# Kernel tuning notes

Hardware: AMD Instinct MI355X
Metric: run time of the kernel (lower is better)

Reference implementation:

```python
import jax, jax.numpy as jnp
import numpy as np

DIM = 768
HEADS = 12


def setup_inputs() -> dict:
    key = jax.random.key(0)
    ks = jax.random.split(key, 7)
    bs, nmm, nv, na = 32, 256, 196, 60
    s = DIM ** -0.5
    return {
        "xmm": jax.random.normal(ks[0], (bs, nmm, DIM), jnp.float32),
        "xv": jax.random.normal(ks[1], (bs, nv, DIM), jnp.float32),
        "xa": jax.random.normal(ks[2], (bs, na, DIM), jnp.float32),
        "Wq": jax.random.normal(ks[3], (DIM, DIM), jnp.float32) * s,
        "Wkv": jax.random.normal(ks[4], (DIM, 2 * DIM), jnp.float32) * s,
        "Wproj": jax.random.normal(ks[5], (DIM, DIM), jnp.float32) * s,
        "bproj": jnp.zeros((DIM,), jnp.float32),
    }


def reference(xmm, xv, xa, Wq, Wkv, Wproj, bproj):
    bs, nmm, dim = xmm.shape
    hd = dim // HEADS
    scale = hd ** -0.5
    x_src = jnp.concatenate([xv, xa], axis=1)            # [bs, nv+na, dim]
    q = (xmm @ Wq).reshape(bs, nmm, HEADS, hd).transpose(0, 2, 1, 3)   # [b,h,q,d]
    kv = (x_src @ Wkv).reshape(bs, -1, 2, HEADS, hd).transpose(2, 0, 3, 1, 4)
    k, v = kv[0], kv[1]                                  # [b,h,k,d]
    attn = jax.nn.softmax(jnp.einsum('bhqd,bhkd->bhqk', q, k) * scale, axis=-1)
    out = jnp.einsum('bhqk,bhkd->bhqd', attn, v)
    out = out.transpose(0, 2, 1, 3).reshape(bs, nmm, dim)
    out = out @ Wproj + bproj
    return out, attn
```

## Files before the change

### kernel.cpp

```cpp
#include <hip/hip_runtime.h>


typedef __attribute__((ext_vector_type(8))) _Float16 f16x8;
typedef __attribute__((ext_vector_type(4))) _Float16 f16x4;
typedef __attribute__((ext_vector_type(4))) float    f32x4;

#define AS1 __attribute__((address_space(1)))
#define AS3 __attribute__((address_space(3)))

__device__ __forceinline__ void gload_lds16(const void* g, void* l) {
    void* gnc = const_cast<void*>(g);
    __builtin_amdgcn_global_load_lds((AS1 void*)gnc, (AS3 void*)l, 16, 0, 0);
}

__global__ __launch_bounds__(256) void cast_f32_f16(const float* __restrict__ in,
                                                    _Float16* __restrict__ out, int n4) {
    int id = blockIdx.x * 256 + threadIdx.x;
    if (id >= n4) return;
    float4 v = ((const float4*)in)[id];
    f16x4 h = { (_Float16)v.x, (_Float16)v.y, (_Float16)v.z, (_Float16)v.w };
    ((f16x4*)out)[id] = h;
}

__global__ __launch_bounds__(256) void concat_cast(const float* __restrict__ xv,
                                                   const float* __restrict__ xa,
                                                   _Float16* __restrict__ out) {
    int id = blockIdx.x * 256 + threadIdx.x;
    if (id >= 1572864) return;
    int c4 = id % 192;
    int r  = (id / 192) & 255;
    int b  = id / 49152;
    float4 v;
    if (r < 196) v = ((const float4*)xv)[((long)b * 196 + r) * 192 + c4];
    else         v = ((const float4*)xa)[((long)b * 60 + (r - 196)) * 192 + c4];
    f16x4 h = { (_Float16)v.x, (_Float16)v.y, (_Float16)v.z, (_Float16)v.w };
    ((f16x4*)out)[id] = h;
}

__global__ __launch_bounds__(256) void transcast(const float* __restrict__ in,
                                                 _Float16* __restrict__ out, int K, int N) {
    int id = blockIdx.x * 256 + threadIdx.x;
    if (id >= K * N) return;
    int k = id % K, n = id / K;
    out[id] = (_Float16)in[(long)k * N + n];
}

template <int OUT_F32>
__global__ __launch_bounds__(256, 2)
void gemm_bt(const _Float16* __restrict__ A, const _Float16* __restrict__ Bt,
             void* __restrict__ C, const float* __restrict__ bias,
             int M, int N, int K) {
    __shared__ _Float16 As[128 * 64];
    __shared__ _Float16 Bs[128 * 64];

    const int tid  = threadIdx.x;
    const int wave = tid >> 6, lane = tid & 63;
    const int lrow = lane & 15, quad = lane >> 4;
    const long bm = (long)blockIdx.y * 128, bn = (long)blockIdx.x * 128;
    const int wm = (wave >> 1) * 64, wn = (wave & 1) * 64;

    f32x4 acc[4][4];
    const f32x4 fz = {0.f, 0.f, 0.f, 0.f};
#pragma unroll
    for (int mt = 0; mt < 4; ++mt)
#pragma unroll
        for (int nt = 0; nt < 4; ++nt) acc[mt][nt] = fz;

    for (int k0 = 0; k0 < K; k0 += 64) {
#pragma unroll
        for (int it = 0; it < 4; ++it) {
            int seg = tid + it * 256;
            int rr = seg >> 3, pp = seg & 7;
            int cc = ((pp ^ (rr & 7)) << 3);
            gload_lds16(A  + (bm + rr) * (long)K + k0 + cc, As + seg * 8);
            gload_lds16(Bt + (bn + rr) * (long)K + k0 + cc, Bs + seg * 8);
        }
        __syncthreads();
#pragma unroll
        for (int ks = 0; ks < 2; ++ks) {
            f16x8 af[4], bf[4];
#pragma unroll
            for (int mt = 0; mt < 4; ++mt) {
                int r = wm + mt * 16 + lrow;
                af[mt] = *(const f16x8*)(As + r * 64 + (((ks * 4 + quad) ^ (r & 7)) << 3));
            }
#pragma unroll
            for (int nt = 0; nt < 4; ++nt) {
                int r = wn + nt * 16 + lrow;
                bf[nt] = *(const f16x8*)(Bs + r * 64 + (((ks * 4 + quad) ^ (r & 7)) << 3));
            }
#pragma unroll
            for (int mt = 0; mt < 4; ++mt)
#pragma unroll
                for (int nt = 0; nt < 4; ++nt)
                    acc[mt][nt] = __builtin_amdgcn_mfma_f32_16x16x32_f16(
                        af[mt], bf[nt], acc[mt][nt], 0, 0, 0);
        }
        __syncthreads();
    }

#pragma unroll
    for (int mt = 0; mt < 4; ++mt) {
#pragma unroll
        for (int j = 0; j < 4; ++j) {
            long row = bm + wm + mt * 16 + quad * 4 + j;
#pragma unroll
            for (int nt = 0; nt < 4; ++nt) {
                long col = bn + wn + nt * 16 + lrow;
                float v = acc[mt][nt][j];
                if (OUT_F32) ((float*)C)[row * N + col] = v + bias[col];
                else         ((_Float16*)C)[row * N + col] = (_Float16)v;
            }
        }
    }
}

__global__ __launch_bounds__(256, 2)
void attn_kernel(const _Float16* __restrict__ Qg, const _Float16* __restrict__ KVg,
                 float* __restrict__ attn_out, _Float16* __restrict__ Og) {
    __shared__ _Float16 sh[32768];
    _Float16* Ks = sh;
    _Float16* Vt = sh + 16384;
    _Float16* Ps = sh;

    const int tid  = threadIdx.x;
    const int wave = tid >> 6, lane = tid & 63;
    const int lrow = lane & 15, quad = lane >> 4;
    const int qb = blockIdx.x, h = blockIdx.y, b = blockIdx.z;
    const long qrow0 = (long)b * 256 + qb * 64;
    const long krow0 = (long)b * 256;

    f16x8 aq[2];
#pragma unroll
    for (int ks = 0; ks < 2; ++ks)
        aq[ks] = *(const f16x8*)(Qg + (qrow0 + wave * 16 + lrow) * 768 + h * 64 + ks * 32 + quad * 8);

#pragma unroll
    for (int it = 0; it < 8; ++it) {
        int seg = tid + it * 256;
        int rr = seg >> 3, pp = seg & 7;
        int cc = ((pp ^ (rr & 7)) << 3);
        gload_lds16(KVg + (krow0 + rr) * 1536 + h * 64 + cc, Ks + seg * 8);
    }
#pragma unroll
    for (int it = 0; it < 8; ++it) {
        int seg = tid + it * 256;
        int key = seg >> 3, d0 = (seg & 7) * 8;
        f16x8 v = *(const f16x8*)(KVg + (krow0 + key) * 1536 + 768 + h * 64 + d0);
#pragma unroll
        for (int i = 0; i < 8; ++i) {
            int d = d0 + i;
            Vt[d * 256 + ((((key >> 3) ^ (d & 7)) << 3) | (key & 7))] = v[i];
        }
    }
    __syncthreads();

    f32x4 sacc[16];
    const f32x4 fz = {0.f, 0.f, 0.f, 0.f};
#pragma unroll
    for (int nt = 0; nt < 16; ++nt) sacc[nt] = fz;
#pragma unroll
    for (int ks = 0; ks < 2; ++ks) {
#pragma unroll
        for (int nt = 0; nt < 16; ++nt) {
            int r = nt * 16 + lrow;
            f16x8 bk = *(const f16x8*)(Ks + r * 64 + (((ks * 4 + quad) ^ (r & 7)) << 3));
            sacc[nt] = __builtin_amdgcn_mfma_f32_16x16x32_f16(aq[ks], bk, sacc[nt], 0, 0, 0);
        }
    }

    float li[4];
#pragma unroll
    for (int j = 0; j < 4; ++j) {
        float m = -1e30f;
#pragma unroll
        for (int nt = 0; nt < 16; ++nt) { sacc[nt][j] *= 0.125f; m = fmaxf(m, sacc[nt][j]); }
        m = fmaxf(m, __shfl_xor(m, 1));
        m = fmaxf(m, __shfl_xor(m, 2));
        m = fmaxf(m, __shfl_xor(m, 4));
        m = fmaxf(m, __shfl_xor(m, 8));
        float s = 0.f;
#pragma unroll
        for (int nt = 0; nt < 16; ++nt) {
            float p = __expf(sacc[nt][j] - m);
            sacc[nt][j] = p; s += p;
        }
        s += __shfl_xor(s, 1); s += __shfl_xor(s, 2);
        s += __shfl_xor(s, 4); s += __shfl_xor(s, 8);
        li[j] = 1.f / s;
    }
    __syncthreads();

    const long abase = (((long)b * 12 + h) * 256 + qb * 64) * 256;
#pragma unroll
    for (int j = 0; j < 4; ++j) {
        int prow = wave * 16 + quad * 4 + j;
#pragma unroll
        for (int nt = 0; nt < 16; ++nt) {
            int col = nt * 16 + lrow;
            float p = sacc[nt][j];
            Ps[prow * 256 + ((((col >> 3) ^ (prow & 7)) << 3) | (col & 7))] = (_Float16)p;
            attn_out[abase + (long)prow * 256 + col] = p * li[j];
        }
    }
    __syncthreads();

    f32x4 oacc[4];
#pragma unroll
    for (int nt = 0; nt < 4; ++nt) oacc[nt] = fz;
#pragma unroll
    for (int ks = 0; ks < 8; ++ks) {
        int pr = wave * 16 + lrow;
        f16x8 ap = *(const f16x8*)(Ps + pr * 256 + (((ks * 4 + quad) ^ (pr & 7)) << 3));
#pragma unroll
        for (int nt = 0; nt < 4; ++nt) {
            int d = nt * 16 + lrow;
            f16x8 bv = *(const f16x8*)(Vt + d * 256 + (((ks * 4 + quad) ^ (d & 7)) << 3));
            oacc[nt] = __builtin_amdgcn_mfma_f32_16x16x32_f16(ap, bv, oacc[nt], 0, 0, 0);
        }
    }
#pragma unroll
    for (int j = 0; j < 4; ++j) {
        long orow = qrow0 + wave * 16 + quad * 4 + j;
#pragma unroll
        for (int nt = 0; nt < 4; ++nt)
            Og[orow * 768 + h * 64 + nt * 16 + lrow] = (_Float16)(oacc[nt][j] * li[j]);
    }
}

extern "C" void kernel_launch(void* const* d_in, const int* in_sizes, int n_in,
                              void* d_out, int out_size, void* d_ws, size_t ws_size,
                              hipStream_t stream) {
    const float* xmm   = (const float*)d_in[0];
    const float* xv    = (const float*)d_in[1];
    const float* xa    = (const float*)d_in[2];
    const float* Wq    = (const float*)d_in[3];
    const float* Wkv   = (const float*)d_in[4];
    const float* Wproj = (const float*)d_in[5];
    const float* bproj = (const float*)d_in[6];

    float* out  = (float*)d_out;
    float* attn = out + 6291456;

    char* ws = (char*)d_ws;
    _Float16* xmm16  = (_Float16*)(ws);
    _Float16* xsrc16 = (_Float16*)(ws + 12582912);
    _Float16* WqT    = (_Float16*)(ws + 25165824);
    _Float16* WkvT   = (_Float16*)(ws + 26345472);
    _Float16* WprojT = (_Float16*)(ws + 28704768);
    _Float16* Q16    = (_Float16*)(ws + 29884416);
    _Float16* KV16   = (_Float16*)(ws + 42467328);
    _Float16* O16    = xmm16;

    cast_f32_f16<<<6144, 256, 0, stream>>>(xmm, xmm16, 1572864);
    concat_cast <<<6144, 256, 0, stream>>>(xv, xa, xsrc16);
    transcast   <<<2304, 256, 0, stream>>>(Wq,    WqT,    768, 768);
    transcast   <<<4608, 256, 0, stream>>>(Wkv,   WkvT,   768, 1536);
    transcast   <<<2304, 256, 0, stream>>>(Wproj, WprojT, 768, 768);

    gemm_bt<0><<<dim3(6, 64),  256, 0, stream>>>(xmm16,  WqT,  (void*)Q16,  nullptr, 8192, 768,  768);
    gemm_bt<0><<<dim3(12, 64), 256, 0, stream>>>(xsrc16, WkvT, (void*)KV16, nullptr, 8192, 1536, 768);

    attn_kernel<<<dim3(4, 12, 32), 256, 0, stream>>>(Q16, KV16, attn, O16);

    gemm_bt<1><<<dim3(6, 64),  256, 0, stream>>>(O16, WprojT, (void*)out, bproj, 8192, 768, 768);
}
```

Before: 310.2 us.

## Merge prep and QKV launches, swap MFMA operands for vectorized epilogue stores

Folds the five cast and transpose kernels into two launches and merges the Q and KV GEMMs into a single grid, reducing launch count and tail effects. It swaps the MFMA A/B operands so each lane holds four consecutive columns, which allows float4 and f16x4 stores in the GEMM epilogues, the attention probability writes and the output writes, instead of scalar strided stores. The softmax scale of 0.125 is folded into the transposed Wq weights. Row reductions now use two cross-lane shuffles instead of four. P is now rounded to fp16 after normalization, which changes numerics slightly.

```diff
diff --git a/kernel.cpp b/kernel.cpp
--- a/kernel.cpp
+++ b/kernel.cpp
@@ -13,50 +13,68 @@
     __builtin_amdgcn_global_load_lds((AS1 void*)gnc, (AS3 void*)l, 16, 0, 0);
 }
 
-__global__ __launch_bounds__(256) void cast_f32_f16(const float* __restrict__ in,
-                                                    _Float16* __restrict__ out, int n4) {
+__global__ __launch_bounds__(256) void prep_acts(const float* __restrict__ xmm,
+                                                 const float* __restrict__ xv,
+                                                 const float* __restrict__ xa,
+                                                 _Float16* __restrict__ xmm16,
+                                                 _Float16* __restrict__ xsrc16) {
     int id = blockIdx.x * 256 + threadIdx.x;
-    if (id >= n4) return;
-    float4 v = ((const float4*)in)[id];
+    float4 v;
+    _Float16* dst;
+    int off;
+    if (id < 1572864) {
+        v = ((const float4*)xmm)[id];
+        dst = xmm16; off = id;
+    } else {
+        int t = id - 1572864;
+        int c4 = t % 192;
+        int r  = (t / 192) & 255;
+        int b  = t / 49152;
+        if (r < 196) v = ((const float4*)xv)[((long)b * 196 + r) * 192 + c4];
+        else         v = ((const float4*)xa)[((long)b * 60 + (r - 196)) * 192 + c4];
+        dst = xsrc16; off = t;
+    }
     f16x4 h = { (_Float16)v.x, (_Float16)v.y, (_Float16)v.z, (_Float16)v.w };
-    ((f16x4*)out)[id] = h;
-}
-
-__global__ __launch_bounds__(256) void concat_cast(const float* __restrict__ xv,
-                                                   const float* __restrict__ xa,
-                                                   _Float16* __restrict__ out) {
+    ((f16x4*)dst)[off] = h;
+}
+
+__global__ __launch_bounds__(256) void prep_weights(const float* __restrict__ Wq,
+                                                    const float* __restrict__ Wkv,
+                                                    const float* __restrict__ Wproj,
+                                                    _Float16* __restrict__ WqT,
+                                                    _Float16* __restrict__ WkvT,
+                                                    _Float16* __restrict__ WprojT) {
     int id = blockIdx.x * 256 + threadIdx.x;
-    if (id >= 1572864) return;
-    int c4 = id % 192;
-    int r  = (id / 192) & 255;
-    int b  = id / 49152;
-    float4 v;
-    if (r < 196) v = ((const float4*)xv)[((long)b * 196 + r) * 192 + c4];
-    else         v = ((const float4*)xa)[((long)b * 60 + (r - 196)) * 192 + c4];
-    f16x4 h = { (_Float16)v.x, (_Float16)v.y, (_Float16)v.z, (_Float16)v.w };
-    ((f16x4*)out)[id] = h;
-}
-
-__global__ __launch_bounds__(256) void transcast(const float* __restrict__ in,
-                                                 _Float16* __restrict__ out, int K, int N) {
-    int id = blockIdx.x * 256 + threadIdx.x;
-    if (id >= K * N) return;
-    int k = id % K, n = id / K;
-    out[id] = (_Float16)in[(long)k * N + n];
+    if (id < 589824) {
+        int k = id % 768, n = id / 768;
+        WqT[id] = (_Float16)(0.125f * Wq[(long)k * 768 + n]);
+        return;
+    }
+    id -= 589824;
+    if (id < 1179648) {
+        int k = id % 768, n = id / 768;
+        WkvT[id] = (_Float16)Wkv[(long)k * 1536 + n];
+        return;
+    }
+    id -= 1179648;
+    if (id < 589824) {
+        int k = id % 768, n = id / 768;
+        WprojT[id] = (_Float16)Wproj[(long)k * 768 + n];
+    }
 }
 
 template <int OUT_F32>
-__global__ __launch_bounds__(256, 2)
-void gemm_bt(const _Float16* __restrict__ A, const _Float16* __restrict__ Bt,
-             void* __restrict__ C, const float* __restrict__ bias,
-             int M, int N, int K) {
+__device__ __forceinline__ void gemm_body(const _Float16* __restrict__ A,
+                                          const _Float16* __restrict__ Bt,
+                                          void* __restrict__ C,
+                                          const float* __restrict__ bias,
+                                          long bm, long bn, int N, int K) {
     __shared__ _Float16 As[128 * 64];
     __shared__ _Float16 Bs[128 * 64];
 
     const int tid  = threadIdx.x;
     const int wave = tid >> 6, lane = tid & 63;
     const int lrow = lane & 15, quad = lane >> 4;
-    const long bm = (long)blockIdx.y * 128, bn = (long)blockIdx.x * 128;
     const int wm = (wave >> 1) * 64, wn = (wave & 1) * 64;
 
     f32x4 acc[4][4];
@@ -94,25 +112,45 @@
 #pragma unroll
                 for (int nt = 0; nt < 4; ++nt)
                     acc[mt][nt] = __builtin_amdgcn_mfma_f32_16x16x32_f16(
-                        af[mt], bf[nt], acc[mt][nt], 0, 0, 0);
+                        bf[nt], af[mt], acc[mt][nt], 0, 0, 0);
         }
         __syncthreads();
     }
 
 #pragma unroll
     for (int mt = 0; mt < 4; ++mt) {
-#pragma unroll
-        for (int j = 0; j < 4; ++j) {
-            long row = bm + wm + mt * 16 + quad * 4 + j;
-#pragma unroll
-            for (int nt = 0; nt < 4; ++nt) {
-                long col = bn + wn + nt * 16 + lrow;
-                float v = acc[mt][nt][j];
-                if (OUT_F32) ((float*)C)[row * N + col] = v + bias[col];
-                else         ((_Float16*)C)[row * N + col] = (_Float16)v;
+        long row = bm + wm + mt * 16 + lrow;
+#pragma unroll
+        for (int nt = 0; nt < 4; ++nt) {
+            long col0 = bn + wn + nt * 16 + quad * 4;
+            if (OUT_F32) {
+                float4 b4 = *(const float4*)(bias + col0);
+                float4 o = { acc[mt][nt][0] + b4.x, acc[mt][nt][1] + b4.y,
+                             acc[mt][nt][2] + b4.z, acc[mt][nt][3] + b4.w };
+                *(float4*)((float*)C + row * N + col0) = o;
+            } else {
+                f16x4 h = { (_Float16)acc[mt][nt][0], (_Float16)acc[mt][nt][1],
+                            (_Float16)acc[mt][nt][2], (_Float16)acc[mt][nt][3] };
+                *(f16x4*)((_Float16*)C + row * N + col0) = h;
             }
         }
     }
+}
+
+__global__ __launch_bounds__(256, 2)
+void gemm_qkv(const _Float16* __restrict__ xmm16, const _Float16* __restrict__ xsrc16,
+              const _Float16* __restrict__ WqT, const _Float16* __restrict__ WkvT,
+              _Float16* __restrict__ Q16, _Float16* __restrict__ KV16) {
+    const int bx = blockIdx.x;
+    const long bm = (long)blockIdx.y * 128;
+    if (bx < 6) gemm_body<0>(xmm16,  WqT,  (void*)Q16,  nullptr, bm, (long)bx * 128,       768,  768);
+    else        gemm_body<0>(xsrc16, WkvT, (void*)KV16, nullptr, bm, (long)(bx - 6) * 128, 1536, 768);
+}
+
+__global__ __launch_bounds__(256, 2)
+void gemm_proj(const _Float16* __restrict__ O16, const _Float16* __restrict__ WprojT,
+               float* __restrict__ out, const float* __restrict__ bias) {
+    gemm_body<1>(O16, WprojT, (void*)out, bias, (long)blockIdx.y * 128, (long)blockIdx.x * 128, 768, 768);
 }
 
 __global__ __launch_bounds__(256, 2)
@@ -165,43 +203,40 @@
         for (int nt = 0; nt < 16; ++nt) {
             int r = nt * 16 + lrow;
             f16x8 bk = *(const f16x8*)(Ks + r * 64 + (((ks * 4 + quad) ^ (r & 7)) << 3));
-            sacc[nt] = __builtin_amdgcn_mfma_f32_16x16x32_f16(aq[ks], bk, sacc[nt], 0, 0, 0);
-        }
-    }
-
-    float li[4];
-#pragma unroll
-    for (int j = 0; j < 4; ++j) {
-        float m = -1e30f;
-#pragma unroll
-        for (int nt = 0; nt < 16; ++nt) { sacc[nt][j] *= 0.125f; m = fmaxf(m, sacc[nt][j]); }
-        m = fmaxf(m, __shfl_xor(m, 1));
-        m = fmaxf(m, __shfl_xor(m, 2));
-        m = fmaxf(m, __shfl_xor(m, 4));
-        m = fmaxf(m, __shfl_xor(m, 8));
-        float s = 0.f;
-#pragma unroll
-        for (int nt = 0; nt < 16; ++nt) {
+            sacc[nt] = __builtin_amdgcn_mfma_f32_16x16x32_f16(bk, aq[ks], sacc[nt], 0, 0, 0);
+        }
+    }
+
+    float m = -1e30f;
+#pragma unroll
+    for (int nt = 0; nt < 16; ++nt)
+#pragma unroll
+        for (int j = 0; j < 4; ++j) m = fmaxf(m, sacc[nt][j]);
+    m = fmaxf(m, __shfl_xor(m, 16));
+    m = fmaxf(m, __shfl_xor(m, 32));
+    float s = 0.f;
+#pragma unroll
+    for (int nt = 0; nt < 16; ++nt)
+#pragma unroll
+        for (int j = 0; j < 4; ++j) {
             float p = __expf(sacc[nt][j] - m);
             sacc[nt][j] = p; s += p;
         }
-        s += __shfl_xor(s, 1); s += __shfl_xor(s, 2);
-        s += __shfl_xor(s, 4); s += __shfl_xor(s, 8);
-        li[j] = 1.f / s;
-    }
+    s += __shfl_xor(s, 16);
+    s += __shfl_xor(s, 32);
+    const float li = 1.f / s;
+
     __syncthreads();
 
     const long abase = (((long)b * 12 + h) * 256 + qb * 64) * 256;
-#pragma unroll
-    for (int j = 0; j < 4; ++j) {
-        int prow = wave * 16 + quad * 4 + j;
-#pragma unroll
-        for (int nt = 0; nt < 16; ++nt) {
-            int col = nt * 16 + lrow;
-            float p = sacc[nt][j];
-            Ps[prow * 256 + ((((col >> 3) ^ (prow & 7)) << 3) | (col & 7))] = (_Float16)p;
-            attn_out[abase + (long)prow * 256 + col] = p * li[j];
-        }
+    const int q = wave * 16 + lrow;
+#pragma unroll
+    for (int nt = 0; nt < 16; ++nt) {
+        float4 o = { sacc[nt][0] * li, sacc[nt][1] * li, sacc[nt][2] * li, sacc[nt][3] * li };
+        *(float4*)(attn_out + abase + (long)q * 256 + nt * 16 + quad * 4) = o;
+        f16x4 hp = { (_Float16)o.x, (_Float16)o.y, (_Float16)o.z, (_Float16)o.w };
+        int blk = nt * 2 + (quad >> 1);
+        *(f16x4*)(Ps + q * 256 + ((blk ^ (q & 7)) << 3) + ((quad & 1) << 2)) = hp;
     }
     __syncthreads();
 
@@ -216,15 +251,14 @@
         for (int nt = 0; nt < 4; ++nt) {
             int d = nt * 16 + lrow;
             f16x8 bv = *(const f16x8*)(Vt + d * 256 + (((ks * 4 + quad) ^ (d & 7)) << 3));
-            oacc[nt] = __builtin_amdgcn_mfma_f32_16x16x32_f16(ap, bv, oacc[nt], 0, 0, 0);
-        }
-    }
-#pragma unroll
-    for (int j = 0; j < 4; ++j) {
-        long orow = qrow0 + wave * 16 + quad * 4 + j;
-#pragma unroll
-        for (int nt = 0; nt < 4; ++nt)
-            Og[orow * 768 + h * 64 + nt * 16 + lrow] = (_Float16)(oacc[nt][j] * li[j]);
+            oacc[nt] = __builtin_amdgcn_mfma_f32_16x16x32_f16(bv, ap, oacc[nt], 0, 0, 0);
+        }
+    }
+#pragma unroll
+    for (int nt = 0; nt < 4; ++nt) {
+        f16x4 ho = { (_Float16)oacc[nt][0], (_Float16)oacc[nt][1],
+                     (_Float16)oacc[nt][2], (_Float16)oacc[nt][3] };
+        *(f16x4*)(Og + (qrow0 + wave * 16 + lrow) * 768 + h * 64 + nt * 16 + quad * 4) = ho;
     }
 }
 
@@ -252,16 +286,12 @@
     _Float16* KV16   = (_Float16*)(ws + 42467328);
     _Float16* O16    = xmm16;
 
-    cast_f32_f16<<<6144, 256, 0, stream>>>(xmm, xmm16, 1572864);
-    concat_cast <<<6144, 256, 0, stream>>>(xv, xa, xsrc16);
-    transcast   <<<2304, 256, 0, stream>>>(Wq,    WqT,    768, 768);
-    transcast   <<<4608, 256, 0, stream>>>(Wkv,   WkvT,   768, 1536);
-    transcast   <<<2304, 256, 0, stream>>>(Wproj, WprojT, 768, 768);
-
-    gemm_bt<0><<<dim3(6, 64),  256, 0, stream>>>(xmm16,  WqT,  (void*)Q16,  nullptr, 8192, 768,  768);
-    gemm_bt<0><<<dim3(12, 64), 256, 0, stream>>>(xsrc16, WkvT, (void*)KV16, nullptr, 8192, 1536, 768);
+    prep_acts   <<<12288, 256, 0, stream>>>(xmm, xv, xa, xmm16, xsrc16);
+    prep_weights<<<9216,  256, 0, stream>>>(Wq, Wkv, Wproj, WqT, WkvT, WprojT);
+
+    gemm_qkv<<<dim3(18, 64), 256, 0, stream>>>(xmm16, xsrc16, WqT, WkvT, Q16, KV16);
 
     attn_kernel<<<dim3(4, 12, 32), 256, 0, stream>>>(Q16, KV16, attn, O16);
 
-    gemm_bt<1><<<dim3(6, 64),  256, 0, stream>>>(O16, WprojT, (void*)out, bproj, 8192, 768, 768);
-}
+    gemm_proj<<<dim3(6, 64), 256, 0, stream>>>(O16, WprojT, out, bproj);
+}
```

Measured after the change: 298.9 us. 1.04x faster.
